# Performance work log

Measured on AMD Instinct MI355X. Metric: run time of the kernel, lower is better.

## Reference

```python
import jax, jax.numpy as jnp
import numpy as np

POOLED_H = 8      # init: pooled_height
POOLED_W = 64     # init: pooled_width
SPATIAL_SCALE = 1.0  # init: spatial_scale


def setup_inputs() -> dict:
    key = jax.random.key(0)
    k1, k2, k3, k4, k5, k6, k7 = jax.random.split(key, 7)
    B, C, H, W = 4, 256, 160, 160
    N = 512
    features = jax.random.normal(k1, (B, C, H, W), dtype=jnp.float32)
    # rois: [batch_idx, cx, cy, h, w, theta]
    bidx = jax.random.randint(k2, (N,), 0, B).astype(jnp.float32)
    cx = jax.random.uniform(k3, (N,), minval=32.0, maxval=W - 32.0)
    cy = jax.random.uniform(k4, (N,), minval=16.0, maxval=H - 16.0)
    h = jax.random.uniform(k5, (N,), minval=8.0, maxval=32.0)
    w = jax.random.uniform(k6, (N,), minval=32.0, maxval=128.0)
    theta = jax.random.uniform(k7, (N,), minval=-0.5, maxval=0.5)
    rois = jnp.stack([bidx, cx, cy, h, w, theta], axis=1).astype(jnp.float32)
    return {"features": features, "rois": rois}


def _rroi_align(features, rois, ph_out, pw_out, scale):
    B, C, H, W = features.shape
    bidx = rois[:, 0].astype(jnp.int32)
    cx = rois[:, 1] * scale
    cy = rois[:, 2] * scale
    rh = rois[:, 3] * scale
    rw = rois[:, 4] * scale
    theta = rois[:, 5]

    # bin-center offsets in roi-local coordinates (origin at roi center)
    px = jnp.arange(pw_out, dtype=jnp.float32) + 0.5 - pw_out / 2.0  # [PW]
    py = jnp.arange(ph_out, dtype=jnp.float32) + 0.5 - ph_out / 2.0  # [PH]
    sx = rw / pw_out  # [N] bin width
    sy = rh / ph_out  # [N] bin height
    xx = px[None, None, :] * sx[:, None, None]  # [N,1,PW]
    yy = py[None, :, None] * sy[:, None, None]  # [N,PH,1]
    ct = jnp.cos(theta)[:, None, None]
    st = jnp.sin(theta)[:, None, None]
    # rotate roi-local bin centers into image coords (affine transform)
    x = ct * xx + st * yy + cx[:, None, None]   # [N,PH,PW]
    y = -st * xx + ct * yy + cy[:, None, None]  # [N,PH,PW]

    x0 = jnp.floor(x)
    y0 = jnp.floor(y)
    lx = x - x0  # bilinear weights
    ly = y - y0
    x0i = x0.astype(jnp.int32)
    y0i = y0.astype(jnp.int32)

    feat = features.reshape(B, C, H * W)

    def gather(yi, xi):
        valid = (yi >= 0) & (yi < H) & (xi >= 0) & (xi < W)
        idx = jnp.clip(yi, 0, H - 1) * W + jnp.clip(xi, 0, W - 1)
        # advanced indexing -> [N,PH,PW,C]
        v = feat[bidx[:, None, None], :, idx]
        return v * valid[..., None].astype(feat.dtype)

    v00 = gather(y0i, x0i)
    v01 = gather(y0i, x0i + 1)
    v10 = gather(y0i + 1, x0i)
    v11 = gather(y0i + 1, x0i + 1)

    lx_ = lx[..., None]
    ly_ = ly[..., None]
    out = (v00 * (1 - lx_) * (1 - ly_)
           + v01 * lx_ * (1 - ly_)
           + v10 * (1 - lx_) * ly_
           + v11 * lx_ * ly_)
    return jnp.transpose(out, (0, 3, 1, 2))  # [N,C,PH,PW]


def reference(features, rois):
    return _rroi_align(features, rois, POOLED_H, POOLED_W, SPATIAL_SCALE)
```

## Files before the change

### kernel.cpp

```cpp
#include <hip/hip_runtime.h>
#include <math.h>

#define RR_B  4
#define RR_C  256
#define RR_H  160
#define RR_W  160
#define RR_PH 8
#define RR_PW 64
#define RR_N  512
#define RR_HW (RR_H * RR_W)

typedef float    f32x4_v __attribute__((ext_vector_type(4)));
typedef _Float16 f16x4_v __attribute__((ext_vector_type(4)));

__device__ __forceinline__ unsigned short f32_to_bf16(float f) {
    const unsigned u = __float_as_uint(f);
    return (unsigned short)((u + 0x7FFFu + ((u >> 16) & 1u)) >> 16);
}
__device__ __forceinline__ float bf16_to_f32(unsigned short h) {
    return __uint_as_float(((unsigned)h) << 16);
}
__device__ __forceinline__ float4 ld_bf4(const unsigned short* p) {
    const ushort4 u = *(const ushort4*)p;
    return make_float4(bf16_to_f32(u.x), bf16_to_f32(u.y),
                       bf16_to_f32(u.z), bf16_to_f32(u.w));
}

__global__ __launch_bounds__(256) void transpose_kernel(
    const float* __restrict__ in,
    unsigned short* __restrict__ outT)
{
    __shared__ float tile[64][65];

    const int blk = blockIdx.x;
    const int b   = blk / 1600;
    const int rem = blk % 1600;
    const int hw0 = (rem >> 2) << 6;
    const int c0  = (rem & 3) << 6;

    const int tx = threadIdx.x & 63;
    const int ty = threadIdx.x >> 6;

    const float* src = in + ((size_t)b * RR_C) * RR_HW;
    unsigned short* dst = outT + ((size_t)b * RR_HW) * RR_C;

    #pragma unroll
    for (int i = 0; i < 16; ++i) {
        const int cl = i * 4 + ty;
        tile[cl][tx] = src[(size_t)(c0 + cl) * RR_HW + hw0 + tx];
    }
    __syncthreads();
    #pragma unroll
    for (int i = 0; i < 16; ++i) {
        const int hl = i * 4 + ty;
        dst[(size_t)(hw0 + hl) * RR_C + c0 + tx] = f32_to_bf16(tile[tx][hl]);
    }
}

__global__ __launch_bounds__(256) void rroi_gather_kernel(
    const unsigned short* __restrict__ featT,
    const float* __restrict__ rois,
    float* __restrict__ out)
{
    __shared__ f16x4_v tile4[256 * 8];

    const int phys = blockIdx.x;
    const int blk  = (phys & 7) * 1024 + (phys >> 3);
    const int n    = blk >> 4;
    const int py   = (blk >> 1) & 7;
    const int half = blk & 1;
    const int tid  = threadIdx.x;
    const int lane = tid & 63;
    const int pxg  = tid >> 6;
    const int c0   = lane << 2;

    const float* r = rois + n * 6;
    const int   b     = min(max((int)r[0], 0), RR_B - 1);
    const float cx    = r[1];
    const float cy    = r[2];
    const float rh    = r[3];
    const float rw    = r[4];
    const float theta = r[5];

    const float sxs = rw * (1.0f / RR_PW);
    const float sys = rh * (1.0f / RR_PH);
    const float ct = cosf(theta);
    const float st = sinf(theta);
    const float yy = ((float)py + 0.5f - RR_PH * 0.5f) * sys;

    const unsigned short* fb = featT + (size_t)b * RR_HW * RR_C + c0;
    float* obase = out + ((size_t)n * RR_C) * (RR_PH * RR_PW)
                       + (size_t)py * RR_PW;

    #pragma unroll
    for (int px4loc = 0; px4loc < 2; ++px4loc) {
        const int q = px4loc * 4 + pxg;
        const int pxbase = half * 32 + q * 4;
        float4 v[4];
        #pragma unroll
        for (int k = 0; k < 4; ++k) {
            const int px = pxbase + k;
            const float xx = ((float)px + 0.5f - RR_PW * 0.5f) * sxs;
            const float x  =  ct * xx + st * yy + cx;
            const float y  = -st * xx + ct * yy + cy;
            const float x0f = floorf(x);
            const float y0f = floorf(y);
            const float lx = x - x0f;
            const float ly = y - y0f;
            const int x0i = (int)x0f;
            const int y0i = (int)y0f;
            const int x1i = x0i + 1;
            const int y1i = y0i + 1;
            const bool vx0 = (x0i >= 0) && (x0i < RR_W);
            const bool vx1 = (x1i >= 0) && (x1i < RR_W);
            const bool vy0 = (y0i >= 0) && (y0i < RR_H);
            const bool vy1 = (y1i >= 0) && (y1i < RR_H);
            const int cxi0 = min(max(x0i, 0), RR_W - 1);
            const int cxi1 = min(max(x1i, 0), RR_W - 1);
            const int cyi0 = min(max(y0i, 0), RR_H - 1);
            const int cyi1 = min(max(y1i, 0), RR_H - 1);
            const float w00 = (1.0f - lx) * (1.0f - ly) * ((vx0 && vy0) ? 1.0f : 0.0f);
            const float w01 = lx          * (1.0f - ly) * ((vx1 && vy0) ? 1.0f : 0.0f);
            const float w10 = (1.0f - lx) * ly          * ((vx0 && vy1) ? 1.0f : 0.0f);
            const float w11 = lx          * ly          * ((vx1 && vy1) ? 1.0f : 0.0f);

            const float4 v00 = ld_bf4(fb + (size_t)(cyi0 * RR_W + cxi0) * RR_C);
            const float4 v01 = ld_bf4(fb + (size_t)(cyi0 * RR_W + cxi1) * RR_C);
            const float4 v10 = ld_bf4(fb + (size_t)(cyi1 * RR_W + cxi0) * RR_C);
            const float4 v11 = ld_bf4(fb + (size_t)(cyi1 * RR_W + cxi1) * RR_C);

            v[k].x = w00 * v00.x + w01 * v01.x + w10 * v10.x + w11 * v11.x;
            v[k].y = w00 * v00.y + w01 * v01.y + w10 * v10.y + w11 * v11.y;
            v[k].z = w00 * v00.z + w01 * v01.z + w10 * v10.z + w11 * v11.z;
            v[k].w = w00 * v00.w + w01 * v01.w + w10 * v10.w + w11 * v11.w;
        }
        f16x4_v s0, s1, s2, s3;
        s0.x = (_Float16)v[0].x; s0.y = (_Float16)v[1].x; s0.z = (_Float16)v[2].x; s0.w = (_Float16)v[3].x;
        s1.x = (_Float16)v[0].y; s1.y = (_Float16)v[1].y; s1.z = (_Float16)v[2].y; s1.w = (_Float16)v[3].y;
        s2.x = (_Float16)v[0].z; s2.y = (_Float16)v[1].z; s2.z = (_Float16)v[2].z; s2.w = (_Float16)v[3].z;
        s3.x = (_Float16)v[0].w; s3.y = (_Float16)v[1].w; s3.z = (_Float16)v[2].w; s3.w = (_Float16)v[3].w;
        const int qs = q ^ (lane & 7);
        tile4[(c0 + 0) * 8 + qs] = s0;
        tile4[(c0 + 1) * 8 + qs] = s1;
        tile4[(c0 + 2) * 8 + qs] = s2;
        tile4[(c0 + 3) * 8 + qs] = s3;
    }
    __syncthreads();
    float* oh = obase + half * 32;
    #pragma unroll
    for (int it = 0; it < 8; ++it) {
        const int ch = it * 32 + (tid >> 3);
        const int q  = tid & 7;
        const int qs = q ^ ((ch >> 2) & 7);
        const f16x4_v hv = tile4[ch * 8 + qs];
        f32x4_v nv;
        nv.x = (float)hv.x; nv.y = (float)hv.y; nv.z = (float)hv.z; nv.w = (float)hv.w;
        __builtin_nontemporal_store(
            nv, (f32x4_v*)(oh + (size_t)ch * (RR_PH * RR_PW) + q * 4));
    }
}

__global__ __launch_bounds__(256) void rroi_align_fallback(
    const float* __restrict__ features,
    const float* __restrict__ rois,
    float* __restrict__ out)
{
    const int blk = blockIdx.x;
    const int n  = blk >> 3;
    const int py = blk & 7;
    const int px = threadIdx.x & 63;
    const int cc = threadIdx.x >> 6;

    const float* r = rois + n * 6;
    const int   b     = min(max((int)r[0], 0), RR_B - 1);
    const float cx    = r[1];
    const float cy    = r[2];
    const float rh    = r[3];
    const float rw    = r[4];
    const float theta = r[5];

    const float sxs = rw * (1.0f / RR_PW);
    const float sys = rh * (1.0f / RR_PH);
    const float xx = ((float)px + 0.5f - RR_PW * 0.5f) * sxs;
    const float yy = ((float)py + 0.5f - RR_PH * 0.5f) * sys;
    const float ct = cosf(theta);
    const float st = sinf(theta);
    const float x = ct * xx + st * yy + cx;
    const float y = -st * xx + ct * yy + cy;
    const float x0f = floorf(x);
    const float y0f = floorf(y);
    const float lx = x - x0f;
    const float ly = y - y0f;
    const int x0i = (int)x0f;
    const int y0i = (int)y0f;
    const int x1i = x0i + 1;
    const int y1i = y0i + 1;
    const bool vx0 = (x0i >= 0) && (x0i < RR_W);
    const bool vx1 = (x1i >= 0) && (x1i < RR_W);
    const bool vy0 = (y0i >= 0) && (y0i < RR_H);
    const bool vy1 = (y1i >= 0) && (y1i < RR_H);
    const int cx0 = min(max(x0i, 0), RR_W - 1);
    const int cx1 = min(max(x1i, 0), RR_W - 1);
    const int cy0 = min(max(y0i, 0), RR_H - 1);
    const int cy1 = min(max(y1i, 0), RR_H - 1);
    const float w00 = (1.0f - lx) * (1.0f - ly) * ((vx0 && vy0) ? 1.0f : 0.0f);
    const float w01 = lx          * (1.0f - ly) * ((vx1 && vy0) ? 1.0f : 0.0f);
    const float w10 = (1.0f - lx) * ly          * ((vx0 && vy1) ? 1.0f : 0.0f);
    const float w11 = lx          * ly          * ((vx1 && vy1) ? 1.0f : 0.0f);
    const int o00 = cy0 * RR_W + cx0;
    const int o01 = cy0 * RR_W + cx1;
    const int o10 = cy1 * RR_W + cx0;
    const int o11 = cy1 * RR_W + cx1;
    const size_t plane = (size_t)RR_HW;
    const float* base = features + (size_t)b * RR_C * plane + (size_t)cc * plane;
    float* op = out + (size_t)n * RR_C * (RR_PH * RR_PW)
                    + (size_t)cc * (RR_PH * RR_PW)
                    + (size_t)py * RR_PW + px;
    #pragma unroll 4
    for (int c = cc; c < RR_C; c += 4) {
        const float v00 = base[o00];
        const float v01 = base[o01];
        const float v10 = base[o10];
        const float v11 = base[o11];
        *op = w00 * v00 + w01 * v01 + w10 * v10 + w11 * v11;
        base += 4 * plane;
        op   += 4 * (RR_PH * RR_PW);
    }
}

extern "C" void kernel_launch(void* const* d_in, const int* in_sizes, int n_in,
                              void* d_out, int out_size, void* d_ws, size_t ws_size,
                              hipStream_t stream) {
    const float* features = (const float*)d_in[0];
    const float* rois     = (const float*)d_in[1];
    float* out = (float*)d_out;

    const size_t needed = (size_t)RR_B * RR_HW * RR_C * sizeof(unsigned short);

    if (ws_size >= needed) {
        unsigned short* featT = (unsigned short*)d_ws;
        hipLaunchKernelGGL(transpose_kernel, dim3(RR_B * 400 * 4), dim3(256), 0,
                           stream, features, featT);
        hipLaunchKernelGGL(rroi_gather_kernel, dim3(RR_N * RR_PH * 2), dim3(256), 0,
                           stream, featT, rois, out);
    } else {
        hipLaunchKernelGGL(rroi_align_fallback, dim3(RR_N * RR_PH), dim3(256), 0,
                           stream, features, rois, out);
    }
}
```

Measured before the change: 381.2 us.

## Sort ROIs by batch and spatial cell to improve gather cache locality

Adds a single-block bitonic sort kernel that orders ROIs by batch index and coarse 8-pixel cell of the center, then has the gather kernel process ROIs in that order. Neighbouring blocks then tend to read overlapping regions of the transposed feature map, which should raise L2/MALL hit rates for the bilinear gathers. It costs one extra small kernel launch and an indirection load per block.

Result: faster. 360.5 us (-5.4%).

```diff
diff --git a/kernel.cpp b/kernel.cpp
--- a/kernel.cpp
+++ b/kernel.cpp
@@ -26,6 +26,35 @@
                        bf16_to_f32(u.z), bf16_to_f32(u.w));
 }
 
+__global__ __launch_bounds__(512) void roi_sort_kernel(
+    const float* __restrict__ rois, int* __restrict__ order)
+{
+    __shared__ unsigned skey[RR_N];
+    const int t = threadIdx.x;
+    {
+        const float* r = rois + t * 6;
+        const int b   = min(max((int)r[0], 0), RR_B - 1);
+        const int cyc = min(max((int)(r[2] * 0.125f), 0), 31);
+        const int cxc = min(max((int)(r[1] * 0.125f), 0), 31);
+        skey[t] = ((unsigned)b << 19) | ((unsigned)cyc << 14)
+                | ((unsigned)cxc << 9) | (unsigned)t;
+    }
+    __syncthreads();
+    for (int k = 2; k <= RR_N; k <<= 1) {
+        for (int j = k >> 1; j > 0; j >>= 1) {
+            const int ixj = t ^ j;
+            if (ixj > t) {
+                const bool asc = ((t & k) == 0);
+                const unsigned a = skey[t];
+                const unsigned c = skey[ixj];
+                if ((a > c) == asc) { skey[t] = c; skey[ixj] = a; }
+            }
+            __syncthreads();
+        }
+    }
+    order[t] = (int)(skey[t] & 511u);
+}
+
 __global__ __launch_bounds__(256) void transpose_kernel(
     const float* __restrict__ in,
     unsigned short* __restrict__ outT)
@@ -60,13 +89,14 @@
 __global__ __launch_bounds__(256) void rroi_gather_kernel(
     const unsigned short* __restrict__ featT,
     const float* __restrict__ rois,
+    const int* __restrict__ order,
     float* __restrict__ out)
 {
     __shared__ f16x4_v tile4[256 * 8];
 
     const int phys = blockIdx.x;
     const int blk  = (phys & 7) * 1024 + (phys >> 3);
-    const int n    = blk >> 4;
+    const int n    = order[blk >> 4];
     const int py   = (blk >> 1) & 7;
     const int half = blk & 1;
     const int tid  = threadIdx.x;
@@ -235,14 +265,18 @@
     const float* rois     = (const float*)d_in[1];
     float* out = (float*)d_out;
 
-    const size_t needed = (size_t)RR_B * RR_HW * RR_C * sizeof(unsigned short);
+    const size_t featT_bytes = (size_t)RR_B * RR_HW * RR_C * sizeof(unsigned short);
+    const size_t needed = featT_bytes + RR_N * sizeof(int);
 
     if (ws_size >= needed) {
         unsigned short* featT = (unsigned short*)d_ws;
+        int* order = (int*)((char*)d_ws + featT_bytes);
         hipLaunchKernelGGL(transpose_kernel, dim3(RR_B * 400 * 4), dim3(256), 0,
                            stream, features, featT);
+        hipLaunchKernelGGL(roi_sort_kernel, dim3(1), dim3(RR_N), 0,
+                           stream, rois, order);
         hipLaunchKernelGGL(rroi_gather_kernel, dim3(RR_N * RR_PH * 2), dim3(256), 0,
-                           stream, featT, rois, out);
+                           stream, featT, rois, order, out);
     } else {
         hipLaunchKernelGGL(rroi_align_fallback, dim3(RR_N * RR_PH), dim3(256), 0,
                            stream, features, rois, out);
```
